# Performance work log

Hardware: AMD Instinct MI355X
Metric: run time of the kernel (lower is better)

The kernel has to match this reference:

```python
import jax, jax.numpy as jnp
import numpy as np

B, S, D = 4, 2048, 1024  # batch, seq_len (= context_length), d_in = d_out


def setup_inputs() -> dict:
    key = jax.random.key(0)
    k0, k1, k2, k3 = jax.random.split(key, 4)
    scale = 1.0 / np.sqrt(D)  # keep activations well-scaled
    return {
        "x": jax.random.normal(k0, (B, S, D), dtype=jnp.float32),
        "Wq": jax.random.normal(k1, (D, D), dtype=jnp.float32) * scale,
        "Wk": jax.random.normal(k2, (D, D), dtype=jnp.float32) * scale,
        "Wv": jax.random.normal(k3, (D, D), dtype=jnp.float32) * scale,
    }


def reference(x, Wq, Wk, Wv):
    # Linear projections (torch Linear with bias=False == x @ W^T; here weights
    # are stored pre-transposed as [d_in, d_out]).
    q = jnp.einsum("bsd,de->bse", x, Wq)
    k = jnp.einsum("bsd,de->bse", x, Wk)
    v = jnp.einsum("bsd,de->bse", x, Wv)

    d_k = k.shape[-1]
    scores = jnp.einsum("bqd,bkd->bqk", q, k) / jnp.sqrt(jnp.float32(d_k))

    # Causal mask: disallow attending to future tokens (strict upper triangle).
    n = x.shape[1]
    causal = jnp.tril(jnp.ones((n, n), dtype=bool))  # True = allowed
    scores = jnp.where(causal[None, :, :], scores, -jnp.inf)

    attn = jax.nn.softmax(scores, axis=-1)
    # dropout_ratio = 0.0 -> identity (eval-mode equivalent)
    return jnp.einsum("bqk,bkd->bqd", attn, v)
```

## Files before the change

kernel.cpp:

```cpp
#include <hip/hip_runtime.h>
#include <math.h>


typedef float  f32x4  __attribute__((ext_vector_type(4)));
typedef int    i32x4  __attribute__((ext_vector_type(4)));
typedef __bf16 bf16x8 __attribute__((ext_vector_type(8)));

__device__ inline ushort f2bf(float f) {
    union { float f; unsigned u; } a; a.f = f;
    unsigned u = a.u;
    return (ushort)((u + 0x7fffu + ((u >> 16) & 1u)) >> 16);
}
__device__ inline bf16x8 as_bf(i32x4 v) {
    union { i32x4 i; bf16x8 b; } u; u.i = v; return u.b;
}

#define GLDS(gp, lp)                                                         \
    __builtin_amdgcn_global_load_lds(                                        \
        (const __attribute__((address_space(1))) void*)(gp),                 \
        (__attribute__((address_space(3))) void*)(lp), 16, 0, 0)

#define BKK 32

__device__ inline int swz(int row, int c) { return c ^ ((row >> 1) & 3); }

template <int BMT, int BNT, int MODE, int OUT>
__global__ __launch_bounds__((BMT / 64) * (BNT / 64) * 64,
                             ((BMT / 64) * (BNT / 64) == 8) ? 4 : 3)
void gemm_bf16(
    const ushort* __restrict__ A, const ushort* __restrict__ B0,
    float* __restrict__ Cf, ushort* __restrict__ Cb, ushort* __restrict__ Vt,
    int N, int K, int lda, int ldb,
    long long sA, long long sB, long long sC, float alpha)
{
    constexpr int NWC = BNT / 64;
    constexpr int T   = (BMT / 64) * NWC * 64;
    constexpr int RPG = T / 4;
    constexpr int IA  = BMT / RPG;
    constexpr int IB  = BNT / RPG;
    constexpr int L   = IA + IB;
    static_assert(L == 3 || L == 4, "gate literals cover L=3,4");

    __shared__ ushort SH[3 * BMT * BKK + 3 * BNT * BKK];
#define ASB(bi) (SH + (bi) * (BMT * BKK))
#define BSB(bi) (SH + 3 * (BMT * BKK) + (bi) * (BNT * BKK))

    A  += (long long)blockIdx.z * sA;
    B0 += (long long)blockIdx.z * sB;

    int byi = blockIdx.y;
    if (MODE != 0) byi = gridDim.y - 1 - byi;

    const int m0 = byi * BMT;
    const int n0 = blockIdx.x * BNT;
    if (MODE == 1 && n0 > m0 + (BMT - 1)) return;
    int kend = K;
    if (MODE == 2) kend = min(K, m0 + BMT);

    const int tid = threadIdx.x;
    const int l   = tid & 63;
    const int w   = tid >> 6;
    const int g   = l >> 4;
    const int r16 = l & 15;
    const int wr  = w / NWC, wc = w % NWC;

    f32x4 acc[4][4];
#pragma unroll
    for (int mi = 0; mi < 4; ++mi)
#pragma unroll
        for (int ni = 0; ni < 4; ++ni)
            acc[mi][ni] = (f32x4){0.f, 0.f, 0.f, 0.f};

    const int srow = w * 16 + (l >> 2);
    const int cg   = swz(srow, l & 3);
    const ushort* gA = A  + (size_t)(m0 + srow) * lda + cg * 8;
    const ushort* gB = B0 + (size_t)(n0 + srow) * ldb + cg * 8;

#define STAGE(bi, k0)                                                        \
    do {                                                                     \
        _Pragma("unroll")                                                    \
        for (int ia = 0; ia < IA; ++ia)                                      \
            GLDS(gA + (k0) + (size_t)(ia * RPG) * lda,                       \
                 ASB(bi) + (ia * RPG + w * 16) * BKK);                       \
        _Pragma("unroll")                                                    \
        for (int ib = 0; ib < IB; ++ib)                                      \
            GLDS(gB + (k0) + (size_t)(ib * RPG) * ldb,                       \
                 BSB(bi) + (ib * RPG + w * 16) * BKK);                       \
    } while (0)

    const int nt = kend / BKK;
    STAGE(0, 0);
    if (nt > 1) STAGE(1, BKK);

    int cur = 0;
    for (int t = 0; t < nt; ++t) {
        if (t + 1 < nt) {
            if constexpr (L == 3)
                asm volatile("s_waitcnt vmcnt(3)" ::: "memory");
            else
                asm volatile("s_waitcnt vmcnt(4)" ::: "memory");
        } else {
            asm volatile("s_waitcnt vmcnt(0)" ::: "memory");
        }
        __builtin_amdgcn_s_barrier();
        asm volatile("" ::: "memory");

        const int nxt = (cur >= 1) ? cur - 1 : 2;
        if (t + 2 < nt) STAGE(nxt, (t + 2) * BKK);

        const ushort* Ab = ASB(cur);
        const ushort* Bb = BSB(cur);
        i32x4 av[4], bv[4];
#pragma unroll
        for (int mi = 0; mi < 4; ++mi) {
            const int r = wr * 64 + mi * 16 + r16;
            av[mi] = *(const i32x4*)(Ab + r * BKK + swz(r, g) * 8);
        }
#pragma unroll
        for (int ni = 0; ni < 4; ++ni) {
            const int r = wc * 64 + ni * 16 + r16;
            bv[ni] = *(const i32x4*)(Bb + r * BKK + swz(r, g) * 8);
        }

        __builtin_amdgcn_s_setprio(1);
#pragma unroll
        for (int mi = 0; mi < 4; ++mi)
#pragma unroll
            for (int ni = 0; ni < 4; ++ni)
                acc[mi][ni] = __builtin_amdgcn_mfma_f32_16x16x32_bf16(
                    as_bf(av[mi]), as_bf(bv[ni]), acc[mi][ni], 0, 0, 0);
        __builtin_amdgcn_s_setprio(0);

        asm volatile("" ::: "memory");
        cur = (cur == 2) ? 0 : cur + 1;
    }
#undef STAGE

    if constexpr (OUT == 1) {
        if (n0 >= 2048) {
            ushort* Tb = SH;
            __builtin_amdgcn_s_barrier();
            asm volatile("" ::: "memory");
#pragma unroll
            for (int mi = 0; mi < 4; ++mi) {
#pragma unroll
                for (int ni = 0; ni < 4; ++ni) {
                    const int c0 = wc * 64 + ni * 16 + r16;
                    const int r0 = wr * 64 + mi * 16 + g * 4;
                    ushort4 pk;
                    pk.x = f2bf(acc[mi][ni][0]);
                    pk.y = f2bf(acc[mi][ni][1]);
                    pk.z = f2bf(acc[mi][ni][2]);
                    pk.w = f2bf(acc[mi][ni][3]);
                    *(ushort4*)&Tb[c0 * 136 + r0] = pk;
                }
            }
            asm volatile("" ::: "memory");
            __builtin_amdgcn_s_barrier();
            asm volatile("" ::: "memory");

            const int bb = m0 >> 11, s0 = m0 & 2047;
            const int dl = tid >> 4;
            const int sc = (tid & 15) * 8;
#pragma unroll
            for (int p = 0; p < 8; ++p) {
                const int d = p * 32 + dl;
                const i32x4 v = *(const i32x4*)&Tb[d * 136 + sc];
                *(i32x4*)(Vt + (size_t)bb * 2097152
                          + (size_t)(n0 - 2048 + d) * 2048 + s0 + sc) = v;
            }
            return;
        }
#pragma unroll
        for (int mi = 0; mi < 4; ++mi)
#pragma unroll
            for (int ni = 0; ni < 4; ++ni)
#pragma unroll
                for (int rr = 0; rr < 4; ++rr) {
                    const int gr = m0 + wr * 64 + mi * 16 + g * 4 + rr;
                    const int gc = n0 + wc * 64 + ni * 16 + r16;
                    Cb[(size_t)gr * N + gc] = f2bf(acc[mi][ni][rr]);
                }
        return;
    }

#pragma unroll
    for (int mi = 0; mi < 4; ++mi)
#pragma unroll
        for (int ni = 0; ni < 4; ++ni)
#pragma unroll
            for (int rr = 0; rr < 4; ++rr) {
                const int gr = m0 + wr * 64 + mi * 16 + g * 4 + rr;
                const int gc = n0 + wc * 64 + ni * 16 + r16;
                Cf[(long long)blockIdx.z * sC + (size_t)gr * N + gc] =
                    acc[mi][ni][rr] * alpha;
            }
#undef ASB
#undef BSB
}

__global__ __launch_bounds__(256) void softmax_bf16(float* __restrict__ Sc)
{
    const int row = blockIdx.x;
    float* base = Sc + ((size_t)blockIdx.y * 2048 + row) * 2048;
    const int tid = threadIdx.x;
    const int j0  = tid * 8;

    float s[8];
    if (j0 <= row) {
        const float4 a = *(const float4*)(base + j0);
        const float4 b = *(const float4*)(base + j0 + 4);
        s[0] = a.x; s[1] = a.y; s[2] = a.z; s[3] = a.w;
        s[4] = b.x; s[5] = b.y; s[6] = b.z; s[7] = b.w;
#pragma unroll
        for (int i = 0; i < 8; ++i)
            if (j0 + i > row) s[i] = -INFINITY;
    } else {
#pragma unroll
        for (int i = 0; i < 8; ++i) s[i] = -INFINITY;
    }

    __shared__ float red[256];
    float m = -INFINITY;
#pragma unroll
    for (int i = 0; i < 8; ++i) m = fmaxf(m, s[i]);
    red[tid] = m;
    __syncthreads();
    for (int st = 128; st > 0; st >>= 1) {
        if (tid < st) red[tid] = fmaxf(red[tid], red[tid + st]);
        __syncthreads();
    }
    m = red[0];
    __syncthreads();

    float e[8], sum = 0.f;
#pragma unroll
    for (int i = 0; i < 8; ++i) {
        e[i] = (j0 + i <= row) ? __expf(s[i] - m) : 0.f;
        sum += e[i];
    }
    red[tid] = sum;
    __syncthreads();
    for (int st = 128; st > 0; st >>= 1) {
        if (tid < st) red[tid] += red[tid + st];
        __syncthreads();
    }
    const float inv = 1.f / red[0];

    const int wcols = ((row >> 7) + 1) << 7;
    if (j0 < wcols) {
        i32x4 pk;
        pk[0] = (int)((unsigned)f2bf(e[0] * inv) | ((unsigned)f2bf(e[1] * inv) << 16));
        pk[1] = (int)((unsigned)f2bf(e[2] * inv) | ((unsigned)f2bf(e[3] * inv) << 16));
        pk[2] = (int)((unsigned)f2bf(e[4] * inv) | ((unsigned)f2bf(e[5] * inv) << 16));
        pk[3] = (int)((unsigned)f2bf(e[6] * inv) | ((unsigned)f2bf(e[7] * inv) << 16));
        *(i32x4*)((ushort*)base + j0) = pk;
    }
}

__global__ void cvt_x(const float4* __restrict__ x, ushort4* __restrict__ o, int n4)
{
    const int i = blockIdx.x * 256 + threadIdx.x;
    if (i < n4) {
        const float4 f = x[i];
        ushort4 u;
        u.x = f2bf(f.x); u.y = f2bf(f.y); u.z = f2bf(f.z); u.w = f2bf(f.w);
        o[i] = u;
    }
}

__global__ __launch_bounds__(256) void cvt_wt(const float* __restrict__ Wq,
                                              const float* __restrict__ Wk,
                                              const float* __restrict__ Wv,
                                              ushort* __restrict__ Wt3)
{
    const float* W = (blockIdx.z == 0) ? Wq : (blockIdx.z == 1) ? Wk : Wv;
    ushort* Wt = Wt3 + (size_t)blockIdx.z * 1048576;

    __shared__ float t[32][33];
    const int tx = threadIdx.x & 31, ty = threadIdx.x >> 5;
    const int c = blockIdx.x * 32 + tx;
    const int rbase = blockIdx.y * 32;
#pragma unroll
    for (int i = 0; i < 4; ++i)
        t[ty + i * 8][tx] = W[(size_t)(rbase + ty + i * 8) * 1024 + c];
    __syncthreads();
    const int kT = blockIdx.y * 32 + tx;
    const int nT = blockIdx.x * 32;
#pragma unroll
    for (int i = 0; i < 4; ++i)
        Wt[(size_t)(nT + ty + i * 8) * 1024 + kT] = f2bf(t[tx][ty + i * 8]);
}

extern "C" void kernel_launch(void* const* d_in, const int* in_sizes, int n_in,
                              void* d_out, int out_size, void* d_ws, size_t ws_size,
                              hipStream_t stream)
{
    (void)in_sizes; (void)n_in; (void)out_size; (void)ws_size;

    const float* x  = (const float*)d_in[0];
    const float* Wq = (const float*)d_in[1];
    const float* Wk = (const float*)d_in[2];
    const float* Wv = (const float*)d_in[3];
    float* out = (float*)d_out;

    const int NB = 4, S = 2048, D = 1024;
    const long long SD  = (long long)S * D;
    const long long NSD = NB * SD;
    const long long SS  = (long long)S * S;

    ushort* xb   = (ushort*)d_ws;
    ushort* Wt3  = xb   + NSD;
    ushort* QKVb = Wt3  + 3 * (size_t)D * D;
    ushort* Vt   = QKVb + (size_t)NB * S * 3 * D;
    float*  Sc   = (float*)(Vt + NSD);

    dim3 blk(256), blk5(512);

    cvt_x<<<dim3((unsigned)(NSD / 4 / 256)), blk, 0, stream>>>(
        (const float4*)x, (ushort4*)xb, (int)(NSD / 4));
    cvt_wt<<<dim3(32, 32, 3), blk, 0, stream>>>(Wq, Wk, Wv, Wt3);

    dim3 gp(3 * D / 256, (unsigned)(NB * S / 128), 1);
    gemm_bf16<128, 256, 0, 1><<<gp, blk5, 0, stream>>>(
        xb, Wt3, nullptr, QKVb, Vt,
        3 * D, D, D, D, 0, 0, 0, 1.f);

    dim3 gs(S / 256, S / 128, NB);
    gemm_bf16<128, 256, 1, 0><<<gs, blk5, 0, stream>>>(
        QKVb, QKVb + 1024, Sc, nullptr, nullptr,
        S, D, 3 * D, 3 * D, (long long)S * 3 * D, (long long)S * 3 * D,
        SS, 0.03125f);

    softmax_bf16<<<dim3(S, NB), blk, 0, stream>>>(Sc);

    dim3 gv(D / 256, S / 128, NB);
    gemm_bf16<128, 256, 2, 0><<<gv, blk5, 0, stream>>>(
        (const ushort*)Sc, Vt, out, nullptr, nullptr,
        D, S, 2 * S, S, 2 * SS, SD, SD, 1.f);
}
```

Measured before the change: 160.5 us.

## Merge conversion kernels into one launch and swizzle QKV GEMM blocks across XCDs

Merges the x conversion and the weight transpose-conversion into one kernel launch, with the block index range split between the two jobs. This removes one launch and the gap between the two kernels. It also remaps the flat workgroup index of the projection GEMM (OUT==1) so that consecutive tiles fall on the same XCD, aiming for better L2 reuse of shared A and B tiles. The remap assumes the workgroup count is divisible by 8.

Result: no change. 158.2 us (-1.4%).

```diff
diff --git a/kernel.cpp b/kernel.cpp
--- a/kernel.cpp
+++ b/kernel.cpp
@@ -48,11 +48,18 @@
     A  += (long long)blockIdx.z * sA;
     B0 += (long long)blockIdx.z * sB;
 
-    int byi = blockIdx.y;
-    if (MODE != 0) byi = gridDim.y - 1 - byi;
+    int bx = blockIdx.x, byi = blockIdx.y;
+    if (OUT == 1) {
+        const int nwg = (int)(gridDim.x * gridDim.y);
+        int flat = byi * (int)gridDim.x + bx;
+        flat = (flat & 7) * (nwg >> 3) + (flat >> 3);
+        bx  = flat % (int)gridDim.x;
+        byi = flat / (int)gridDim.x;
+    }
+    if (MODE != 0) byi = (int)gridDim.y - 1 - byi;
 
     const int m0 = byi * BMT;
-    const int n0 = blockIdx.x * BNT;
+    const int n0 = bx * BNT;
     if (MODE == 1 && n0 > m0 + (BMT - 1)) return;
     int kend = K;
     if (MODE == 2) kend = min(K, m0 + BMT);
@@ -258,38 +265,41 @@
     }
 }
 
-__global__ void cvt_x(const float4* __restrict__ x, ushort4* __restrict__ o, int n4)
+__global__ __launch_bounds__(256) void cvt_all(
+    const float4* __restrict__ x4, ushort4* __restrict__ xb4,
+    const float* __restrict__ Wq, const float* __restrict__ Wk,
+    const float* __restrict__ Wv, ushort* __restrict__ Wt3)
 {
-    const int i = blockIdx.x * 256 + threadIdx.x;
-    if (i < n4) {
-        const float4 f = x[i];
+    const int b = blockIdx.x;
+    if (b < 8192) {
+        const int i = b * 256 + threadIdx.x;
+        const float4 f = x4[i];
         ushort4 u;
         u.x = f2bf(f.x); u.y = f2bf(f.y); u.z = f2bf(f.z); u.w = f2bf(f.w);
-        o[i] = u;
-    }
-}
-
-__global__ __launch_bounds__(256) void cvt_wt(const float* __restrict__ Wq,
-                                              const float* __restrict__ Wk,
-                                              const float* __restrict__ Wv,
-                                              ushort* __restrict__ Wt3)
-{
-    const float* W = (blockIdx.z == 0) ? Wq : (blockIdx.z == 1) ? Wk : Wv;
-    ushort* Wt = Wt3 + (size_t)blockIdx.z * 1048576;
-
-    __shared__ float t[32][33];
+        xb4[i] = u;
+        return;
+    }
+    const int t  = b - 8192;
+    const int z  = t >> 10;
+    const int r  = t & 1023;
+    const int bxw = r & 31, byw = r >> 5;
+
+    const float* W = (z == 0) ? Wq : (z == 1) ? Wk : Wv;
+    ushort* Wt = Wt3 + (size_t)z * 1048576;
+
+    __shared__ float tle[32][33];
     const int tx = threadIdx.x & 31, ty = threadIdx.x >> 5;
-    const int c = blockIdx.x * 32 + tx;
-    const int rbase = blockIdx.y * 32;
+    const int c = bxw * 32 + tx;
+    const int rbase = byw * 32;
 #pragma unroll
     for (int i = 0; i < 4; ++i)
-        t[ty + i * 8][tx] = W[(size_t)(rbase + ty + i * 8) * 1024 + c];
+        tle[ty + i * 8][tx] = W[(size_t)(rbase + ty + i * 8) * 1024 + c];
     __syncthreads();
-    const int kT = blockIdx.y * 32 + tx;
-    const int nT = blockIdx.x * 32;
+    const int kT = byw * 32 + tx;
+    const int nT = bxw * 32;
 #pragma unroll
     for (int i = 0; i < 4; ++i)
-        Wt[(size_t)(nT + ty + i * 8) * 1024 + kT] = f2bf(t[tx][ty + i * 8]);
+        Wt[(size_t)(nT + ty + i * 8) * 1024 + kT] = f2bf(tle[tx][ty + i * 8]);
 }
 
 extern "C" void kernel_launch(void* const* d_in, const int* in_sizes, int n_in,
@@ -317,9 +327,8 @@
 
     dim3 blk(256), blk5(512);
 
-    cvt_x<<<dim3((unsigned)(NSD / 4 / 256)), blk, 0, stream>>>(
-        (const float4*)x, (ushort4*)xb, (int)(NSD / 4));
-    cvt_wt<<<dim3(32, 32, 3), blk, 0, stream>>>(Wq, Wk, Wv, Wt3);
+    cvt_all<<<dim3(8192 + 3072), blk, 0, stream>>>(
+        (const float4*)x, (ushort4*)xb, Wq, Wk, Wv, Wt3);
 
     dim3 gp(3 * D / 256, (unsigned)(NB * S / 128), 1);
     gemm_bf16<128, 256, 0, 1><<<gp, blk5, 0, stream>>>(
```
